# Performance work log

Hardware: AMD Instinct MI355X
Metric: run time of the kernel (lower is better)

Reference implementation:

```python
import jax, jax.numpy as jnp
import numpy as np

N_EMBD = 512  # scale uses C = n_embd, per original code

def setup_inputs() -> dict:
    key = jax.random.key(0)
    k1, k2, k3, k4 = jax.random.split(key, 4)
    B, T, C, H = 4, 4096, N_EMBD, 64
    x = jax.random.normal(k1, (B, T, C), dtype=jnp.float32)
    # Linear(n_embd, head_size, bias=False); stored as [C, H] for x @ W
    scale = 1.0 / np.sqrt(C)
    Wq = jax.random.normal(k2, (C, H), dtype=jnp.float32) * scale
    Wk = jax.random.normal(k3, (C, H), dtype=jnp.float32) * scale
    Wv = jax.random.normal(k4, (C, H), dtype=jnp.float32) * scale
    return {"x": x, "Wq": Wq, "Wk": Wk, "Wv": Wv}

def reference(x, Wq, Wk, Wv):
    B, T, C = x.shape
    q = jnp.einsum('btc,ch->bth', x, Wq)
    k = jnp.einsum('btc,ch->bth', x, Wk)
    v = jnp.einsum('btc,ch->bth', x, Wv)
    # NOTE: original scales by sqrt(C)=sqrt(n_embd), not sqrt(head_size)
    scores = jnp.einsum('bqh,bkh->bqk', q, k) / jnp.sqrt(jnp.float32(C))
    causal = jnp.tril(jnp.ones((T, T), dtype=bool))
    scores = jnp.where(causal, scores, -jnp.inf)
    weights = jax.nn.softmax(scores, axis=-1)
    out = jnp.einsum('bqk,bkh->bqh', weights, v)
    return out
```

## Files before the change

kernel.cpp:

```cpp
#include <hip/hip_runtime.h>

#define DEV __device__ __forceinline__

typedef __bf16 bf16x8 __attribute__((ext_vector_type(8)));
typedef unsigned short u16x8v __attribute__((ext_vector_type(8)));
typedef float f32x4 __attribute__((ext_vector_type(4)));
typedef float f32x16 __attribute__((ext_vector_type(16)));
typedef unsigned int u32x4v __attribute__((ext_vector_type(4)));
typedef unsigned short u16;
typedef unsigned int u32;

DEV u16 f2bf(float f) {
    u32 u = __builtin_bit_cast(u32, f);
    u = (u + 0x7FFFu + ((u >> 16) & 1u)) >> 16;
    return (u16)u;
}

DEV float bf2f(u16 v) {
    return __builtin_bit_cast(float, (u32)v << 16);
}

DEV bf16x8 ld_bf8(const u16* p) {
    return *reinterpret_cast<const bf16x8*>(p);
}

DEV bf16x8 ld_lds8(const u16* p) {
    ushort4 a = *reinterpret_cast<const ushort4*>(p);
    ushort4 b = *reinterpret_cast<const ushort4*>(p + 4);
    u16x8v o;
    o[0] = a.x; o[1] = a.y; o[2] = a.z; o[3] = a.w;
    o[4] = b.x; o[5] = b.y; o[6] = b.z; o[7] = b.w;
    return __builtin_bit_cast(bf16x8, o);
}

DEV float fexp2(float x) { return __builtin_amdgcn_exp2f(x); }

DEV u32 cvt_pk_bf16(float a, float b) {
    u32 r;
    asm("v_cvt_pk_bf16_f32 %0, %1, %2" : "=v"(r) : "v"(a), "v"(b));
    return r;
}


__global__ __launch_bounds__(256) void prep_kernel(const float* __restrict__ W0,
                                                   const float* __restrict__ W1,
                                                   const float* __restrict__ W2,
                                                   u16* __restrict__ Wt,
                                                   u32* __restrict__ table) {
    const int blk = blockIdx.x;
    if (blk < 384) {
        int idx = blk * 256 + threadIdx.x;
        int w = idx >> 15, rem = idx & 32767, h = rem >> 9, c = rem & 511;
        const float* W = (w == 0) ? W0 : ((w == 1) ? W1 : W2);
        float v = W[c * 64 + h];
        if (w == 0) v *= 0.044194173824159216f * 1.4426950408889634f;
        Wt[idx] = f2bf(v);
    } else {
        int idx = (blk - 384) * 256 + threadIdx.x;
        if (idx < 512) {
            int j = idx >> 4, k = idx & 15;
            int nch = (j >> 2) + 1;
            if (k < nch) {
                int base = 0;
                for (int i = 0; i < j; ++i) base += (i >> 2) + 1;
                table[base + k] = (u32)j | ((u32)k << 16);
            }
        }
    }
}

__global__ __launch_bounds__(64) void proj_kernel(const float* __restrict__ x,
                                                  const u16* __restrict__ Wt,
                                                  u16* __restrict__ Q,
                                                  u16* __restrict__ Kq,
                                                  u16* __restrict__ Vt) {
    __shared__ __align__(16) u16 xs[2][16][40];
    const int lane = threadIdx.x;
    const int lr = lane & 15, lg = lane >> 4;
    const int r0 = blockIdx.x * 16;
    const int u0 = 2 * lane, u1 = 2 * lane + 1;
    const int sr0 = u0 >> 3, sc0 = (u0 & 7) * 4;
    const int sr1 = u1 >> 3, sc1 = (u1 & 7) * 4;

    f32x4 acc[3][4];
#pragma unroll
    for (int m = 0; m < 3; ++m)
#pragma unroll
        for (int b = 0; b < 4; ++b) acc[m][b] = (f32x4){0.f, 0.f, 0.f, 0.f};

    float4 a0, a1;
#define PLOAD(KK)                                                               \
    {   a0 = *reinterpret_cast<const float4*>(x + (size_t)(r0 + sr0) * 512 + (KK) * 32 + sc0); \
        a1 = *reinterpret_cast<const float4*>(x + (size_t)(r0 + sr1) * 512 + (KK) * 32 + sc1); }
#define PSTORE(BUF)                                                             \
    {   ushort4 h0, h1;                                                         \
        h0.x = f2bf(a0.x); h0.y = f2bf(a0.y); h0.z = f2bf(a0.z); h0.w = f2bf(a0.w); \
        h1.x = f2bf(a1.x); h1.y = f2bf(a1.y); h1.z = f2bf(a1.z); h1.w = f2bf(a1.w); \
        *reinterpret_cast<ushort4*>(&xs[BUF][sr0][sc0]) = h0;                   \
        *reinterpret_cast<ushort4*>(&xs[BUF][sr1][sc1]) = h1;  }

    PLOAD(0);
    PSTORE(0);
    PLOAD(1);

    for (int kk = 0; kk < 16; ++kk) {
        const int buf = kk & 1;
        if (kk + 1 < 16) PSTORE(buf ^ 1);
        if (kk + 2 < 16) PLOAD(kk + 2);

        bf16x8 af = ld_bf8(&xs[buf][lr][lg * 8]);
#pragma unroll
        for (int m = 0; m < 3; ++m) {
#pragma unroll
            for (int nt = 0; nt < 4; ++nt) {
                bf16x8 bf = ld_bf8(Wt + m * 32768 + (lr + 16 * nt) * 512 + kk * 32 + lg * 8);
                acc[m][nt] = __builtin_amdgcn_mfma_f32_16x16x32_bf16(af, bf, acc[m][nt], 0, 0, 0);
            }
        }
    }
#undef PLOAD
#undef PSTORE

    const int rw = r0;
#pragma unroll
    for (int nt = 0; nt < 4; ++nt) {
        const int h = lr + 16 * nt;
#pragma unroll
        for (int reg = 0; reg < 4; ++reg) {
            Q[(size_t)(rw + 4 * lg + reg) * 64 + h]  = f2bf(acc[0][nt][reg]);
            Kq[(size_t)(rw + 4 * lg + reg) * 64 + h] = f2bf(acc[1][nt][reg]);
        }
    }
    const int bidx = rw >> 12;
    const int t0 = (rw & 4095) + 4 * lg;
#pragma unroll
    for (int nt = 0; nt < 4; ++nt) {
        const int h = lr + 16 * nt;
        ushort4 hv;
        hv.x = f2bf(acc[2][nt][0]); hv.y = f2bf(acc[2][nt][1]);
        hv.z = f2bf(acc[2][nt][2]); hv.w = f2bf(acc[2][nt][3]);
        *reinterpret_cast<ushort4*>(Vt + ((size_t)(bidx * 64 + h)) * 4096 + t0) = hv;
    }
}

DEV void mask_diag(f32x16& st, int q31, int hi) {
#pragma unroll
    for (int reg = 0; reg < 16; ++reg) {
        const int crow = (reg & 3) + 8 * (reg >> 2) + 4 * hi;
        if (crow > q31) st[reg] = -3.0e38f;
    }
}

DEV float max16(const f32x16& a) {
    float m0 = fmaxf(fmaxf(a[0], a[1]), a[2]);
    float m1 = fmaxf(fmaxf(a[3], a[4]), a[5]);
    float m2 = fmaxf(fmaxf(a[6], a[7]), a[8]);
    float m3 = fmaxf(fmaxf(a[9], a[10]), a[11]);
    float m4 = fmaxf(fmaxf(a[12], a[13]), a[14]);
    float m5 = fmaxf(fmaxf(m0, m1), a[15]);
    float m6 = fmaxf(fmaxf(m2, m3), m4);
    return fmaxf(m5, m6);
}

DEV float expsum(f32x16& st, float m) {
    float r0 = 0.f, r1 = 0.f, r2 = 0.f, r3 = 0.f;
#pragma unroll
    for (int g = 0; g < 4; ++g) {
        float p0 = fexp2(st[4 * g + 0] - m);
        float p1 = fexp2(st[4 * g + 1] - m);
        float p2 = fexp2(st[4 * g + 2] - m);
        float p3 = fexp2(st[4 * g + 3] - m);
        st[4 * g + 0] = p0; st[4 * g + 1] = p1;
        st[4 * g + 2] = p2; st[4 * g + 3] = p3;
        r0 += p0; r1 += p1; r2 += p2; r3 += p3;
    }
    return (r0 + r1) + (r2 + r3);
}

DEV void packP(const f32x16& st, bf16x8& pb0, bf16x8& pb1, int hi) {
    u32 A0 = cvt_pk_bf16(st[0], st[1]),  A1 = cvt_pk_bf16(st[2], st[3]);
    u32 A2 = cvt_pk_bf16(st[4], st[5]),  A3 = cvt_pk_bf16(st[6], st[7]);
    u32 A4 = cvt_pk_bf16(st[8], st[9]),  A5 = cvt_pk_bf16(st[10], st[11]);
    u32 A6 = cvt_pk_bf16(st[12], st[13]), A7 = cvt_pk_bf16(st[14], st[15]);
    u32 e0 = __shfl_xor(hi ? A0 : A2, 32, 64);
    u32 e1 = __shfl_xor(hi ? A1 : A3, 32, 64);
    u32 e2 = __shfl_xor(hi ? A4 : A6, 32, 64);
    u32 e3 = __shfl_xor(hi ? A5 : A7, 32, 64);
    u32x4v w0, w1;
    w0[0] = hi ? e0 : A0;
    w0[1] = hi ? e1 : A1;
    w0[2] = hi ? A2 : e0;
    w0[3] = hi ? A3 : e1;
    w1[0] = hi ? e2 : A4;
    w1[1] = hi ? e3 : A5;
    w1[2] = hi ? A6 : e2;
    w1[3] = hi ? A7 : e3;
    pb0 = __builtin_bit_cast(bf16x8, w0);
    pb1 = __builtin_bit_cast(bf16x8, w1);
}

__global__ __launch_bounds__(256) void attn_part_kernel(const u16* __restrict__ Q,
                                                        const u16* __restrict__ K,
                                                        const u16* __restrict__ Vt,
                                                        const u32* __restrict__ table,
                                                        u16* __restrict__ Opart,
                                                        float* __restrict__ Mpart,
                                                        float* __restrict__ Lpart) {
    __shared__ __align__(16) u16 Ks[2][32][68];
    __shared__ __align__(16) u16 Vs[2][64][36];

    const int tid = threadIdx.x;
    const int wave = tid >> 6, lane = tid & 63;
    const int q31 = lane & 31, hi = lane >> 5;
    const int bid = blockIdx.x;
    const int b = bid & 3;
    const u32 e = table[143 - (bid >> 2)];
    const int j = (int)(e & 0xffff);
    const int c = (int)(e >> 16);
    const int qi = 4 * j + wave;
    const int qr0 = qi * 32;
    const int s0 = c * 16;
    const int s1 = min(4 * j + 4, s0 + 16);
    const int tile = (b << 7) | qi;

    const u16* Qb = Q + (size_t)b * 4096 * 64;
    const u16* Kb = K + (size_t)b * 4096 * 64;
    const u16* Vb = Vt + (size_t)b * 64 * 4096;

    const int kr = tid >> 3, ku = tid & 7;
    const int vd = tid >> 2, vu = tid & 3;
    const u16* ksrc = Kb + (size_t)kr * 64 + ku * 8;
    const u16* vsrc = Vb + (size_t)vd * 4096 + vu * 8;

    bf16x8 qf[4];
#pragma unroll
    for (int kk = 0; kk < 4; ++kk)
        qf[kk] = ld_bf8(Qb + (size_t)(qr0 + q31) * 64 + kk * 16 + hi * 8);

    f32x16 o0, o1;
#pragma unroll
    for (int r = 0; r < 16; ++r) { o0[r] = 0.f; o1[r] = 0.f; }
    float m_run = -1.0e30f, l_run = 0.f;

    ushort4 k0, k1, v0, v1;
    k0 = *reinterpret_cast<const ushort4*>(ksrc + s0 * 2048);
    k1 = *reinterpret_cast<const ushort4*>(ksrc + s0 * 2048 + 4);
    v0 = *reinterpret_cast<const ushort4*>(vsrc + s0 * 32);
    v1 = *reinterpret_cast<const ushort4*>(vsrc + s0 * 32 + 4);
    *reinterpret_cast<ushort4*>(&Ks[0][kr][ku * 8]) = k0;
    *reinterpret_cast<ushort4*>(&Ks[0][kr][ku * 8 + 4]) = k1;
    *reinterpret_cast<ushort4*>(&Vs[0][vd][vu * 8]) = v0;
    *reinterpret_cast<ushort4*>(&Vs[0][vd][vu * 8 + 4]) = v1;
    if (s0 + 1 < s1) {
        k0 = *reinterpret_cast<const ushort4*>(ksrc + (s0 + 1) * 2048);
        k1 = *reinterpret_cast<const ushort4*>(ksrc + (s0 + 1) * 2048 + 4);
        v0 = *reinterpret_cast<const ushort4*>(vsrc + (s0 + 1) * 32);
        v1 = *reinterpret_cast<const ushort4*>(vsrc + (s0 + 1) * 32 + 4);
    }
    __syncthreads();

    for (int s = s0; s < s1; ++s) {
        const int cb = (s - s0) & 1;
        if (s + 1 < s1) {
            *reinterpret_cast<ushort4*>(&Ks[cb ^ 1][kr][ku * 8]) = k0;
            *reinterpret_cast<ushort4*>(&Ks[cb ^ 1][kr][ku * 8 + 4]) = k1;
            *reinterpret_cast<ushort4*>(&Vs[cb ^ 1][vd][vu * 8]) = v0;
            *reinterpret_cast<ushort4*>(&Vs[cb ^ 1][vd][vu * 8 + 4]) = v1;
        }
        if (s + 2 < s1) {
            k0 = *reinterpret_cast<const ushort4*>(ksrc + (s + 2) * 2048);
            k1 = *reinterpret_cast<const ushort4*>(ksrc + (s + 2) * 2048 + 4);
            v0 = *reinterpret_cast<const ushort4*>(vsrc + (s + 2) * 32);
            v1 = *reinterpret_cast<const ushort4*>(vsrc + (s + 2) * 32 + 4);
        }
        if (s <= qi) {
            f32x16 st;
#pragma unroll
            for (int r = 0; r < 16; ++r) st[r] = 0.f;
#pragma unroll
            for (int kk = 0; kk < 4; ++kk) {
                bf16x8 kf = ld_lds8(&Ks[cb][q31][kk * 16 + hi * 8]);
                st = __builtin_amdgcn_mfma_f32_32x32x16_bf16(kf, qf[kk], st, 0, 0, 0);
            }
            if (s == qi) mask_diag(st, q31, hi);

            float pm = max16(st);
            pm = fmaxf(pm, __shfl_xor(pm, 32, 64));
            if (!__all(pm - m_run <= 11.5f)) {
                float mn = fmaxf(m_run, pm);
                float al = fexp2(m_run - mn);
                m_run = mn;
                l_run *= al;
#pragma unroll
                for (int r = 0; r < 16; ++r) { o0[r] *= al; o1[r] *= al; }
            }
            float rs = expsum(st, m_run);
            rs += __shfl_xor(rs, 32, 64);
            l_run += rs;

            bf16x8 p0, p1;
            packP(st, p0, p1, hi);
            bf16x8 va = ld_lds8(&Vs[cb][q31][hi * 8]);
            bf16x8 vb2 = ld_lds8(&Vs[cb][q31][16 + hi * 8]);
            bf16x8 vc = ld_lds8(&Vs[cb][32 + q31][hi * 8]);
            bf16x8 vdq = ld_lds8(&Vs[cb][32 + q31][16 + hi * 8]);
            o0 = __builtin_amdgcn_mfma_f32_32x32x16_bf16(va, p0, o0, 0, 0, 0);
            o0 = __builtin_amdgcn_mfma_f32_32x32x16_bf16(vb2, p1, o0, 0, 0, 0);
            o1 = __builtin_amdgcn_mfma_f32_32x32x16_bf16(vc, p0, o1, 0, 0, 0);
            o1 = __builtin_amdgcn_mfma_f32_32x32x16_bf16(vdq, p1, o1, 0, 0, 0);
        }
        __syncthreads();
    }

    if (s0 <= qi) {
        const size_t base = (size_t)(tile * 16 + c);
        u16* Op = Opart + base * 2048;
#pragma unroll
        for (int reg = 0; reg < 16; ++reg) {
            const int crow = (reg & 3) + 8 * (reg >> 2) + 4 * hi;
            Op[crow * 32 + q31] = f2bf(o0[reg]);
            Op[(32 + crow) * 32 + q31] = f2bf(o1[reg]);
        }
        if (lane < 32) {
            Mpart[base * 32 + lane] = m_run;
            Lpart[base * 32 + lane] = l_run;
        }
    }
}

__global__ __launch_bounds__(256) void merge_kernel(const u16* __restrict__ Opart,
                                                    const float* __restrict__ Mpart,
                                                    const float* __restrict__ Lpart,
                                                    float* __restrict__ out) {
    __shared__ float ld[2][64 * 33];
    const int tile = blockIdx.x;
    const int tid = threadIdx.x;
    const int q = tid >> 3, dg = tid & 7;
    const int qi = tile & 127;
    const int nc = (qi >> 4) + 1;

    float M = -3.0e38f;
    for (int c = 0; c < nc; ++c)
        M = fmaxf(M, Mpart[(tile * 16 + c) * 32 + q]);

    float L = 0.f;
    float acc[8];
#pragma unroll
    for (int j = 0; j < 8; ++j) acc[j] = 0.f;

    const int drow = tid >> 2;
    const int qq = (tid & 3) * 8;

    u16x8v v = reinterpret_cast<const u16x8v*>(Opart + (size_t)(tile * 16) * 2048)[tid];

    for (int c = 0; c < nc; ++c) {
        const size_t base = (size_t)(tile * 16 + c);
        {
            float* dst = &ld[c & 1][drow * 33 + qq];
#pragma unroll
            for (int j = 0; j < 8; ++j) dst[j] = bf2f(v[j]);
        }
        const int cn = (c + 1 < nc) ? c + 1 : c;
        v = reinterpret_cast<const u16x8v*>(Opart + (size_t)(tile * 16 + cn) * 2048)[tid];

        __syncthreads();
        float w = fexp2(Mpart[base * 32 + q] - M);
        L += w * Lpart[base * 32 + q];
        const float* src = &ld[c & 1][0];
#pragma unroll
        for (int j = 0; j < 8; ++j)
            acc[j] += w * src[(dg * 8 + j) * 33 + q];
    }

    const float inv = 1.0f / L;
    float4 r0, r1;
    r0.x = acc[0] * inv; r0.y = acc[1] * inv; r0.z = acc[2] * inv; r0.w = acc[3] * inv;
    r1.x = acc[4] * inv; r1.y = acc[5] * inv; r1.z = acc[6] * inv; r1.w = acc[7] * inv;
    float4* dst = reinterpret_cast<float4*>(out + ((size_t)(tile * 32 + q)) * 64 + dg * 8);
    dst[0] = r0;
    dst[1] = r1;
}

extern "C" void kernel_launch(void* const* d_in, const int* in_sizes, int n_in,
                              void* d_out, int out_size, void* d_ws, size_t ws_size,
                              hipStream_t stream) {
    const float* x  = (const float*)d_in[0];
    const float* Wq = (const float*)d_in[1];
    const float* Wk = (const float*)d_in[2];
    const float* Wv = (const float*)d_in[3];
    float* out = (float*)d_out;

    char* ws = (char*)d_ws;
    const size_t MB = 1024 * 1024;
    u16* Qw  = (u16*)(ws);
    u16* Kw  = (u16*)(ws + 2 * MB);
    u16* Vtw = (u16*)(ws + 4 * MB);
    u16* Wt  = (u16*)(ws + 6 * MB);
    u32* table = (u32*)(ws + 7 * MB);

    u16* Opart = (u16*)(ws + 8 * MB);
    float* Mpart = (float*)(ws + 8 * MB + 32 * MB);
    float* Lpart = Mpart + (size_t)16 * 512 * 32;

    prep_kernel<<<386, 256, 0, stream>>>(Wq, Wk, Wv, Wt, table);
    proj_kernel<<<1024, 64, 0, stream>>>(x, Wt, Qw, Kw, Vtw);
    attn_part_kernel<<<4 * 144, 256, 0, stream>>>(Qw, Kw, Vtw, table, Opart, Mpart, Lpart);
    merge_kernel<<<512, 256, 0, stream>>>(Opart, Mpart, Lpart, out);
}
```

Before: 68.44 us.

## Process two 32-key blocks per iteration with 64-row K/V shared tiles

The attention loop now stages 64 keys and 64 columns of V per shared-memory buffer. Each wave computes two 32x32 score tiles before a single online-softmax max/rescale step and two P·V accumulations. Global loads widen to 16-byte uint4 fetches, and the loop takes half as many iterations, so there are half as many __syncthreads and max/rescale passes per key range. The cost is doubled LDS use and higher register pressure from holding two score tiles at once, which may lower occupancy.

```diff
diff --git a/kernel.cpp b/kernel.cpp
--- a/kernel.cpp
+++ b/kernel.cpp
@@ -31,6 +31,15 @@
     o[0] = a.x; o[1] = a.y; o[2] = a.z; o[3] = a.w;
     o[4] = b.x; o[5] = b.y; o[6] = b.z; o[7] = b.w;
     return __builtin_bit_cast(bf16x8, o);
+}
+
+DEV void st_lds16(u16* p, uint4 v) {
+    u16x8v t = __builtin_bit_cast(u16x8v, v);
+    ushort4 a, b;
+    a.x = t[0]; a.y = t[1]; a.z = t[2]; a.w = t[3];
+    b.x = t[4]; b.y = t[5]; b.z = t[6]; b.w = t[7];
+    *reinterpret_cast<ushort4*>(p) = a;
+    *reinterpret_cast<ushort4*>(p + 4) = b;
 }
 
 DEV float fexp2(float x) { return __builtin_amdgcn_exp2f(x); }
@@ -206,8 +215,8 @@
                                                         u16* __restrict__ Opart,
                                                         float* __restrict__ Mpart,
                                                         float* __restrict__ Lpart) {
-    __shared__ __align__(16) u16 Ks[2][32][68];
-    __shared__ __align__(16) u16 Vs[2][64][36];
+    __shared__ __align__(16) u16 Ks[2][64][68];
+    __shared__ __align__(16) u16 Vs[2][64][68];
 
     const int tid = threadIdx.x;
     const int wave = tid >> 6, lane = tid & 63;
@@ -227,10 +236,23 @@
     const u16* Kb = K + (size_t)b * 4096 * 64;
     const u16* Vb = Vt + (size_t)b * 64 * 4096;
 
-    const int kr = tid >> 3, ku = tid & 7;
-    const int vd = tid >> 2, vu = tid & 3;
-    const u16* ksrc = Kb + (size_t)kr * 64 + ku * 8;
-    const u16* vsrc = Vb + (size_t)vd * 4096 + vu * 8;
+    const int ur = tid >> 3, uc = (tid & 7) * 8;
+    const u16* ksrc0 = Kb + (size_t)ur * 64 + uc;
+    const u16* ksrc1 = Kb + (size_t)(ur + 32) * 64 + uc;
+    const u16* vsrc0 = Vb + (size_t)ur * 4096 + uc;
+    const u16* vsrc1 = Vb + (size_t)(ur + 32) * 4096 + uc;
+
+    uint4 pk0, pk1, pv0, pv1;
+#define LOADPAIR(S)                                                             \
+    {   pk0 = *reinterpret_cast<const uint4*>(ksrc0 + (S) * 2048);              \
+        pk1 = *reinterpret_cast<const uint4*>(ksrc1 + (S) * 2048);              \
+        pv0 = *reinterpret_cast<const uint4*>(vsrc0 + (S) * 32);                \
+        pv1 = *reinterpret_cast<const uint4*>(vsrc1 + (S) * 32);  }
+#define WRITEBUF(B)                                                             \
+    {   st_lds16(&Ks[B][ur][uc], pk0);                                          \
+        st_lds16(&Ks[B][ur + 32][uc], pk1);                                     \
+        st_lds16(&Vs[B][ur][uc], pv0);                                          \
+        st_lds16(&Vs[B][ur + 32][uc], pv1);  }
 
     bf16x8 qf[4];
 #pragma unroll
@@ -242,49 +264,43 @@
     for (int r = 0; r < 16; ++r) { o0[r] = 0.f; o1[r] = 0.f; }
     float m_run = -1.0e30f, l_run = 0.f;
 
-    ushort4 k0, k1, v0, v1;
-    k0 = *reinterpret_cast<const ushort4*>(ksrc + s0 * 2048);
-    k1 = *reinterpret_cast<const ushort4*>(ksrc + s0 * 2048 + 4);
-    v0 = *reinterpret_cast<const ushort4*>(vsrc + s0 * 32);
-    v1 = *reinterpret_cast<const ushort4*>(vsrc + s0 * 32 + 4);
-    *reinterpret_cast<ushort4*>(&Ks[0][kr][ku * 8]) = k0;
-    *reinterpret_cast<ushort4*>(&Ks[0][kr][ku * 8 + 4]) = k1;
-    *reinterpret_cast<ushort4*>(&Vs[0][vd][vu * 8]) = v0;
-    *reinterpret_cast<ushort4*>(&Vs[0][vd][vu * 8 + 4]) = v1;
-    if (s0 + 1 < s1) {
-        k0 = *reinterpret_cast<const ushort4*>(ksrc + (s0 + 1) * 2048);
-        k1 = *reinterpret_cast<const ushort4*>(ksrc + (s0 + 1) * 2048 + 4);
-        v0 = *reinterpret_cast<const ushort4*>(vsrc + (s0 + 1) * 32);
-        v1 = *reinterpret_cast<const ushort4*>(vsrc + (s0 + 1) * 32 + 4);
-    }
+    LOADPAIR(s0);
+    WRITEBUF(0);
+    if (s0 + 2 < s1) LOADPAIR(s0 + 2);
     __syncthreads();
 
-    for (int s = s0; s < s1; ++s) {
-        const int cb = (s - s0) & 1;
-        if (s + 1 < s1) {
-            *reinterpret_cast<ushort4*>(&Ks[cb ^ 1][kr][ku * 8]) = k0;
-            *reinterpret_cast<ushort4*>(&Ks[cb ^ 1][kr][ku * 8 + 4]) = k1;
-            *reinterpret_cast<ushort4*>(&Vs[cb ^ 1][vd][vu * 8]) = v0;
-            *reinterpret_cast<ushort4*>(&Vs[cb ^ 1][vd][vu * 8 + 4]) = v1;
-        }
+    for (int s = s0; s < s1; s += 2) {
+        const int cb = ((s - s0) >> 1) & 1;
         if (s + 2 < s1) {
-            k0 = *reinterpret_cast<const ushort4*>(ksrc + (s + 2) * 2048);
-            k1 = *reinterpret_cast<const ushort4*>(ksrc + (s + 2) * 2048 + 4);
-            v0 = *reinterpret_cast<const ushort4*>(vsrc + (s + 2) * 32);
-            v1 = *reinterpret_cast<const ushort4*>(vsrc + (s + 2) * 32 + 4);
-        }
+            WRITEBUF(cb ^ 1);
+            if (s + 4 < s1) LOADPAIR(s + 4);
+        }
+
         if (s <= qi) {
-            f32x16 st;
-#pragma unroll
-            for (int r = 0; r < 16; ++r) st[r] = 0.f;
+            const bool doB = (s + 1 <= qi);
+            f32x16 stA;
+#pragma unroll
+            for (int r = 0; r < 16; ++r) stA[r] = 0.f;
 #pragma unroll
             for (int kk = 0; kk < 4; ++kk) {
                 bf16x8 kf = ld_lds8(&Ks[cb][q31][kk * 16 + hi * 8]);
-                st = __builtin_amdgcn_mfma_f32_32x32x16_bf16(kf, qf[kk], st, 0, 0, 0);
-            }
-            if (s == qi) mask_diag(st, q31, hi);
-
-            float pm = max16(st);
+                stA = __builtin_amdgcn_mfma_f32_32x32x16_bf16(kf, qf[kk], stA, 0, 0, 0);
+            }
+            if (s == qi) mask_diag(stA, q31, hi);
+            f32x16 stB;
+            if (doB) {
+#pragma unroll
+                for (int r = 0; r < 16; ++r) stB[r] = 0.f;
+#pragma unroll
+                for (int kk = 0; kk < 4; ++kk) {
+                    bf16x8 kf = ld_lds8(&Ks[cb][32 + q31][kk * 16 + hi * 8]);
+                    stB = __builtin_amdgcn_mfma_f32_32x32x16_bf16(kf, qf[kk], stB, 0, 0, 0);
+                }
+                if (s + 1 == qi) mask_diag(stB, q31, hi);
+            }
+
+            float pm = max16(stA);
+            if (doB) pm = fmaxf(pm, max16(stB));
             pm = fmaxf(pm, __shfl_xor(pm, 32, 64));
             if (!__all(pm - m_run <= 11.5f)) {
                 float mn = fmaxf(m_run, pm);
@@ -294,23 +310,39 @@
 #pragma unroll
                 for (int r = 0; r < 16; ++r) { o0[r] *= al; o1[r] *= al; }
             }
-            float rs = expsum(st, m_run);
+            float rs = expsum(stA, m_run);
+            if (doB) rs += expsum(stB, m_run);
             rs += __shfl_xor(rs, 32, 64);
             l_run += rs;
 
             bf16x8 p0, p1;
-            packP(st, p0, p1, hi);
-            bf16x8 va = ld_lds8(&Vs[cb][q31][hi * 8]);
-            bf16x8 vb2 = ld_lds8(&Vs[cb][q31][16 + hi * 8]);
-            bf16x8 vc = ld_lds8(&Vs[cb][32 + q31][hi * 8]);
-            bf16x8 vdq = ld_lds8(&Vs[cb][32 + q31][16 + hi * 8]);
-            o0 = __builtin_amdgcn_mfma_f32_32x32x16_bf16(va, p0, o0, 0, 0, 0);
-            o0 = __builtin_amdgcn_mfma_f32_32x32x16_bf16(vb2, p1, o0, 0, 0, 0);
-            o1 = __builtin_amdgcn_mfma_f32_32x32x16_bf16(vc, p0, o1, 0, 0, 0);
-            o1 = __builtin_amdgcn_mfma_f32_32x32x16_bf16(vdq, p1, o1, 0, 0, 0);
+            packP(stA, p0, p1, hi);
+            {
+                bf16x8 va = ld_lds8(&Vs[cb][q31][hi * 8]);
+                bf16x8 vb2 = ld_lds8(&Vs[cb][q31][16 + hi * 8]);
+                bf16x8 vc = ld_lds8(&Vs[cb][32 + q31][hi * 8]);
+                bf16x8 vd = ld_lds8(&Vs[cb][32 + q31][16 + hi * 8]);
+                o0 = __builtin_amdgcn_mfma_f32_32x32x16_bf16(va, p0, o0, 0, 0, 0);
+                o0 = __builtin_amdgcn_mfma_f32_32x32x16_bf16(vb2, p1, o0, 0, 0, 0);
+                o1 = __builtin_amdgcn_mfma_f32_32x32x16_bf16(vc, p0, o1, 0, 0, 0);
+                o1 = __builtin_amdgcn_mfma_f32_32x32x16_bf16(vd, p1, o1, 0, 0, 0);
+            }
+            if (doB) {
+                packP(stB, p0, p1, hi);
+                bf16x8 va = ld_lds8(&Vs[cb][q31][32 + hi * 8]);
+                bf16x8 vb2 = ld_lds8(&Vs[cb][q31][48 + hi * 8]);
+                bf16x8 vc = ld_lds8(&Vs[cb][32 + q31][32 + hi * 8]);
+                bf16x8 vd = ld_lds8(&Vs[cb][32 + q31][48 + hi * 8]);
+                o0 = __builtin_amdgcn_mfma_f32_32x32x16_bf16(va, p0, o0, 0, 0, 0);
+                o0 = __builtin_amdgcn_mfma_f32_32x32x16_bf16(vb2, p1, o0, 0, 0, 0);
+                o1 = __builtin_amdgcn_mfma_f32_32x32x16_bf16(vc, p0, o1, 0, 0, 0);
+                o1 = __builtin_amdgcn_mfma_f32_32x32x16_bf16(vd, p1, o1, 0, 0, 0);
+            }
         }
         __syncthreads();
     }
+#undef LOADPAIR
+#undef WRITEBUF
 
     if (s0 <= qi) {
         const size_t base = (size_t)(tile * 16 + c);
```

Result: slower. 74.72 us (+9.2%).
